# Performance work log

Measured on AMD Instinct MI355X. Metric: run time of the kernel, lower is better.

## Reference

```python
import jax, jax.numpy as jnp
import numpy as np

DIM, PATCHES, HID, NCLS, NBLK, PS = 384, 196, 1536, 1000, 24, 16

def fq(w, bits=8):
    # symmetric per-tensor fake quantization (dequantized), as in QAT DynamicQLinear
    n = float(2 ** (bits - 1) - 1)
    s = jnp.max(jnp.abs(w)) / n + 1e-8
    q = jnp.clip(jnp.round(w / s), -n - 1.0, n) * s
    return q

def setup_inputs() -> dict:
    key = jax.random.key(0)
    ks = jax.random.split(key, 12)
    d = {}
    d["x"] = jax.random.normal(ks[0], (64, 3, 224, 224), jnp.float32)
    d["conv_w"] = jax.random.normal(ks[1], (DIM, 3, PS, PS), jnp.float32) * 0.02
    d["conv_b"] = jnp.zeros((DIM,), jnp.float32)
    d["norm1_a"] = jnp.ones((NBLK, DIM), jnp.float32)
    d["norm1_b"] = jnp.zeros((NBLK, DIM), jnp.float32)
    d["attn_w"] = jax.random.normal(ks[2], (NBLK, PATCHES, PATCHES), jnp.float32) * 0.02
    d["attn_b"] = jnp.zeros((NBLK, PATCHES), jnp.float32)
    d["gamma1"] = jnp.full((NBLK, DIM), 1e-4, jnp.float32)
    d["norm2_a"] = jnp.ones((NBLK, DIM), jnp.float32)
    d["norm2_b"] = jnp.zeros((NBLK, DIM), jnp.float32)
    d["mlp_w1"] = jax.random.normal(ks[3], (NBLK, HID, DIM), jnp.float32) * 0.02
    d["mlp_b1"] = jnp.zeros((NBLK, HID), jnp.float32)
    d["mlp_w2"] = jax.random.normal(ks[4], (NBLK, DIM, HID), jnp.float32) * 0.02
    d["mlp_b2"] = jnp.zeros((NBLK, DIM), jnp.float32)
    d["gamma2"] = jnp.full((NBLK, DIM), 1e-4, jnp.float32)
    d["norm_a"] = jnp.ones((DIM,), jnp.float32)
    d["norm_b"] = jnp.zeros((DIM,), jnp.float32)
    d["head_w"] = jax.random.normal(ks[5], (NCLS, DIM), jnp.float32) * 0.02
    d["head_b"] = jnp.zeros((NCLS,), jnp.float32)
    return d

def reference(x, conv_w, conv_b, norm1_a, norm1_b, attn_w, attn_b, gamma1,
              norm2_a, norm2_b, mlp_w1, mlp_b1, mlp_w2, mlp_b2, gamma2,
              norm_a, norm_b, head_w, head_b):
    B = x.shape[0]
    # patch embed: quantized 16x16 stride-16 conv, then flatten(2).transpose(1,2)
    h = jax.lax.conv_general_dilated(x, fq(conv_w), (PS, PS), 'VALID',
                                     dimension_numbers=('NCHW', 'OIHW', 'NCHW'))
    h = h + conv_b[None, :, None, None]
    h = h.reshape(B, DIM, PATCHES).transpose(0, 2, 1)  # [B, 196, 384]

    def step(xc, p):
        a1, b1, aw, ab, g1, a2, b2, w1, bb1, w2, bb2, g2 = p
        # affine norm1 (per-channel)
        t = xc * a1 + b1
        # cross-patch linear applied on transposed layout: out[b,q,d] = sum_p t[b,p,d] W[q,p]
        t = jnp.einsum('bpd,qp->bqd', t, fq(aw)) + ab[None, :, None]
        xc = g1 * t + xc
        # affine norm2 + MLP (384 -> 1536 -> 384, exact GELU)
        t = xc * a2 + b2
        t = jax.nn.gelu(jnp.einsum('bpd,hd->bph', t, fq(w1)) + bb1, approximate=False)
        t = jnp.einsum('bph,dh->bpd', t, fq(w2)) + bb2
        xc = g2 * t + xc
        return xc, None

    h, _ = jax.lax.scan(step, h, (norm1_a, norm1_b, attn_w, attn_b, gamma1,
                                  norm2_a, norm2_b, mlp_w1, mlp_b1, mlp_w2, mlp_b2, gamma2))
    h = h * norm_a + norm_b          # final affine norm
    h = h.mean(axis=1)               # mean pool over patches -> [B, 384]
    return h @ fq(head_w).T + head_b  # [B, 1000]
```

## Files before the change

kernel.cpp:

```cpp
#include <hip/hip_runtime.h>

#define DIM 384
#define PATCHES 196
#define HID 1536
#define NBLK 24
#define NPAD 256
#define XROWS (64 * PATCHES)
#define BDCOLS (64 * DIM)
#define XELEMS (XROWS * DIM)
#define ESTRIDE 132

typedef __attribute__((ext_vector_type(8))) short s8v;
typedef __attribute__((ext_vector_type(4))) float f4v;
typedef unsigned char uchar;
typedef long long i64t;

__device__ __forceinline__ short f2bf(float f) {
  unsigned u = __float_as_uint(f);
  u += 0x7FFFu + ((u >> 16) & 1u);
  return (short)(u >> 16);
}

__device__ __forceinline__ float gelu_f(float x) {
  float u2 = 1.5957691216f * (x + 0.044715f * x * x * x);
  return x / (1.0f + __expf(-u2));
}

__device__ __forceinline__ unsigned pk4_fp8(float a, float b, float c, float d) {
  int lo = __builtin_amdgcn_cvt_pk_fp8_f32(a, b, 0, false);
  int full = __builtin_amdgcn_cvt_pk_fp8_f32(c, d, lo, true);
  return (unsigned)full;
}
__device__ __forceinline__ uchar fp8_1(float a) {
  return (uchar)(__builtin_amdgcn_cvt_pk_fp8_f32(a, a, 0, false) & 0xff);
}

__device__ __forceinline__ void gload_lds16(const void* g, void* l) {
  __builtin_amdgcn_global_load_lds((const __attribute__((address_space(1))) void*)g,
                                   (__attribute__((address_space(3))) void*)l, 16, 0, 0);
}

__global__ __launch_bounds__(256)
void absmax_v4(const float* __restrict__ src, int f4per, int blocks_per,
               unsigned* __restrict__ out) {
  int tens = blockIdx.x / blocks_per;
  int sl = blockIdx.x - tens * blocks_per;
  const float4* p = (const float4*)(src + (size_t)tens * f4per * 4);
  float m = 0.f;
  for (int i = sl * 256 + threadIdx.x; i < f4per; i += blocks_per * 256) {
    float4 v = p[i];
    m = fmaxf(m, fmaxf(fmaxf(fabsf(v.x), fabsf(v.y)), fmaxf(fabsf(v.z), fabsf(v.w))));
  }
  __shared__ float red[256];
  red[threadIdx.x] = m;
  __syncthreads();
  for (int s = 128; s > 0; s >>= 1) {
    if ((int)threadIdx.x < s) red[threadIdx.x] = fmaxf(red[threadIdx.x], red[threadIdx.x + s]);
    __syncthreads();
  }
  if (threadIdx.x == 0) atomicMax(out + tens, __float_as_uint(red[0]));
}

__global__ __launch_bounds__(256)
void quant_w(const float* __restrict__ w, short* __restrict__ q,
             const unsigned* __restrict__ sc, int per, int total) {
  int i = blockIdx.x * 256 + threadIdx.x;
  if (i >= total) return;
  int tens = i / per;
  float s = __uint_as_float(sc[tens]) / 127.0f + 1e-8f;
  float v = rintf(w[i] / s);
  v = fminf(fmaxf(v, -128.0f), 127.0f) * s;
  q[i] = f2bf(v);
}

__global__ __launch_bounds__(256)
void quant_fp8(const float* __restrict__ w, unsigned* __restrict__ q,
               const unsigned* __restrict__ sc, int per, int total4) {
  int i = blockIdx.x * 256 + threadIdx.x;
  if (i >= total4) return;
  int e = i << 2;
  int tens = e / per;
  float s = __uint_as_float(sc[tens]) / 127.0f + 1e-8f;
  float4 w4 = *(const float4*)(w + e);
  float a = fminf(fmaxf(rintf(w4.x / s), -128.0f), 127.0f) * s;
  float b = fminf(fmaxf(rintf(w4.y / s), -128.0f), 127.0f) * s;
  float c = fminf(fmaxf(rintf(w4.z / s), -128.0f), 127.0f) * s;
  float d = fminf(fmaxf(rintf(w4.w / s), -128.0f), 127.0f) * s;
  q[i] = pk4_fp8(a, b, c, d);
}

__global__ __launch_bounds__(256)
void quant_attn_fp8(const float* __restrict__ w, unsigned* __restrict__ q,
                    const unsigned* __restrict__ sc) {
  int i = blockIdx.x * 256 + threadIdx.x;
  if (i >= NBLK * PATCHES * NPAD / 4) return;
  int e = i << 2;
  int col = e & (NPAD - 1);
  int rt = e >> 8;
  int row = rt % PATCHES;
  int tens = rt / PATCHES;
  float s = __uint_as_float(sc[tens]) / 127.0f + 1e-8f;
  const float* wr = w + (size_t)tens * PATCHES * PATCHES + (size_t)row * PATCHES;
  float v[4];
#pragma unroll
  for (int k = 0; k < 4; ++k) {
    int c = col + k;
    v[k] = (c < PATCHES) ? fminf(fmaxf(rintf(wr[c] / s), -128.0f), 127.0f) * s : 0.f;
  }
  q[i] = pk4_fp8(v[0], v[1], v[2], v[3]);
}

__global__ __launch_bounds__(256)
void quant_head_v4(const float* __restrict__ w, float* __restrict__ q,
                   const unsigned* __restrict__ sc) {
  int i = blockIdx.x * 256 + threadIdx.x;
  if (i >= 1000 * DIM / 4) return;
  float s = __uint_as_float(sc[0]) / 127.0f + 1e-8f;
  float4 w4 = *(const float4*)(w + (i << 2));
  float4 o;
  o.x = fminf(fmaxf(rintf(w4.x / s), -128.0f), 127.0f) * s;
  o.y = fminf(fmaxf(rintf(w4.y / s), -128.0f), 127.0f) * s;
  o.z = fminf(fmaxf(rintf(w4.z / s), -128.0f), 127.0f) * s;
  o.w = fminf(fmaxf(rintf(w4.w / s), -128.0f), 127.0f) * s;
  *(float4*)(q + (i << 2)) = o;
}

__global__ __launch_bounds__(256)
void im2col_k(const float* __restrict__ x, short* __restrict__ Xa) {
  int idx = blockIdx.x * 256 + threadIdx.x;
  if (idx >= XROWS * 768 / 4) return;
  int e = idx << 2;
  int r = e / 768, k = e - r * 768;
  int b = r / PATCHES, p = r - b * PATCHES;
  int c = k >> 8, rem = k & 255, ii = rem >> 4, j = rem & 15;
  int ph = p / 14, pw = p - ph * 14;
  const float4 v = *(const float4*)(x + (b * 3 + c) * 50176 + (ph * 16 + ii) * 224 + pw * 16 + j);
  short2* o = (short2*)(Xa + e);
  o[0] = make_short2(f2bf(v.x), f2bf(v.y));
  o[1] = make_short2(f2bf(v.z), f2bf(v.w));
}

__global__ __launch_bounds__(256)
void gemm_conv(const short* __restrict__ A, const short* __restrict__ B,
               float* __restrict__ Xres, const float* __restrict__ bias,
               const float* __restrict__ n1a, const float* __restrict__ n1b,
               uchar* __restrict__ Yt) {
  constexpr int TILE_SHORTS = 192 * 64;
  __shared__ char smem[2 * TILE_SHORTS * 2];
  short* buf0 = (short*)smem;
  float* S = (float*)smem;
  const int lda = 768, K = 768;

  const int t = threadIdx.x;
  const int lane = t & 63;
  const int wid = t >> 6;
  const int wr = wid >> 1, wc = wid & 1;

  const int gx = gridDim.x;
  const int nwg = gx * gridDim.y;
  const int orig = blockIdx.y * gx + blockIdx.x;
  const int q = nwg >> 3, rm = nwg & 7;
  const int xc = orig & 7, jj = orig >> 3;
  const int wg = (xc < rm ? xc * (q + 1) : rm * (q + 1) + (xc - rm) * q) + jj;
  const int bx = wg % gx, by = wg / gx;
  const int m0 = by * 64, n0 = bx * 128;

  f4v acc[2][4];
#pragma unroll
  for (int m = 0; m < 2; ++m)
#pragma unroll
    for (int n = 0; n < 4; ++n) acc[m][n] = (f4v){0.f, 0.f, 0.f, 0.f};

  const int srow = t >> 3;
  const int scol = ((t & 7) ^ (srow & 7)) << 3;
  const short* ga[2];
#pragma unroll
  for (int h = 0; h < 2; ++h) ga[h] = A + (size_t)(m0 + h * 32 + srow) * lda + scol;
  const short* gb[4];
#pragma unroll
  for (int j = 0; j < 4; ++j) gb[j] = B + (size_t)(n0 + j * 32 + srow) * lda + scol;
  short* ldst = buf0 + (t & ~63) * 8;

  auto stage = [&](int slot, int kt) {
    const int koff = kt << 6;
    const int boff = slot * TILE_SHORTS;
    gload_lds16(ga[0] + koff, ldst + boff);
    gload_lds16(ga[1] + koff, ldst + boff + 2048);
#pragma unroll
    for (int j = 0; j < 4; ++j)
      gload_lds16(gb[j] + koff, ldst + boff + 4096 + j * 2048);
  };

  const int l15 = lane & 15, lk = lane >> 4, l7 = lane & 7;
  int paoff[2], pboff[2];
#pragma unroll
  for (int ks = 0; ks < 2; ++ks) {
    const int cgx = ((ks << 2) + lk) ^ l7;
    paoff[ks] = (wr * 32 + l15) * 64 + (cgx << 3);
    pboff[ks] = 4096 + (wc * 64 + l15) * 64 + (cgx << 3);
  }

  const int nk = K >> 6;
  stage(0, 0);
  asm volatile("s_waitcnt vmcnt(0)" ::: "memory");
  __builtin_amdgcn_s_barrier();
  for (int kt = 0; kt < nk; ++kt) {
    const int cur = kt & 1;
    if (kt + 1 < nk) stage(cur ^ 1, kt + 1);
    const short* base = buf0 + cur * TILE_SHORTS;
    s8v af[2][2], bfr[4][2];
#pragma unroll
    for (int m = 0; m < 2; ++m)
#pragma unroll
      for (int ks = 0; ks < 2; ++ks) af[m][ks] = *(const s8v*)(base + paoff[ks] + m * 1024);
#pragma unroll
    for (int n = 0; n < 4; ++n)
#pragma unroll
      for (int ks = 0; ks < 2; ++ks) bfr[n][ks] = *(const s8v*)(base + pboff[ks] + n * 1024);
    asm volatile("s_waitcnt lgkmcnt(0)" ::: "memory");
    __builtin_amdgcn_sched_barrier(0);
    __builtin_amdgcn_s_setprio(1);
#pragma unroll
    for (int m = 0; m < 2; ++m)
#pragma unroll
      for (int n = 0; n < 4; ++n)
#pragma unroll
        for (int ks = 0; ks < 2; ++ks)
          acc[m][n] = __builtin_amdgcn_mfma_f32_16x16x32_bf16(af[m][ks], bfr[n][ks], acc[m][n], 0, 0, 0);
    __builtin_amdgcn_s_setprio(0);
    if (kt + 1 < nk) {
      asm volatile("s_waitcnt vmcnt(0)" ::: "memory");
      __builtin_amdgcn_s_barrier();
    }
  }

  const int cb = (wc << 6) + l15;
  const int rl = t >> 3;
  const int c0 = (t & 7) << 4;
#pragma unroll
  for (int m = 0; m < 2; ++m) {
    __syncthreads();
#pragma unroll
    for (int n = 0; n < 4; ++n) {
      int c = cb + n * 16;
#pragma unroll
      for (int j = 0; j < 4; ++j)
        S[((wr << 4) + (lk << 2) + j) * ESTRIDE + c] = acc[m][n][j];
    }
    __syncthreads();
    const int r = m0 + (rl >> 4) * 32 + m * 16 + (rl & 15);
    const int colg = n0 + c0;
    float xn[16];
#pragma unroll
    for (int i = 0; i < 4; ++i) {
      float4 q4 = *(const float4*)(S + rl * ESTRIDE + c0 + i * 4);
      float4 b4 = *(const float4*)(bias + colg + i * 4);
      float4 o4 = make_float4(q4.x + b4.x, q4.y + b4.y, q4.z + b4.z, q4.w + b4.w);
      *(float4*)(Xres + (size_t)r * DIM + colg + i * 4) = o4;
      xn[4 * i] = o4.x; xn[4 * i + 1] = o4.y; xn[4 * i + 2] = o4.z; xn[4 * i + 3] = o4.w;
    }
    int bb = r / PATCHES, p = r - bb * PATCHES;
    uchar* yrow = Yt + ((size_t)(bb * DIM + colg)) * NPAD + p;
#pragma unroll
    for (int i = 0; i < 4; ++i) {
      float4 a4 = *(const float4*)(n1a + colg + i * 4);
      float4 b4 = *(const float4*)(n1b + colg + i * 4);
      yrow[(4 * i + 0) * NPAD] = fp8_1(xn[4 * i] * a4.x + b4.x);
      yrow[(4 * i + 1) * NPAD] = fp8_1(xn[4 * i + 1] * a4.y + b4.y);
      yrow[(4 * i + 2) * NPAD] = fp8_1(xn[4 * i + 2] * a4.z + b4.z);
      yrow[(4 * i + 3) * NPAD] = fp8_1(xn[4 * i + 3] * a4.w + b4.w);
    }
  }
}

template <int EPI, int NKT>
__global__ __launch_bounds__(256)
void gemm8(const uchar* __restrict__ A, int lda8, int Mlim,
           const uchar* __restrict__ B, int ldb8, int K,
           float* __restrict__ Xres, uchar* __restrict__ OutB8,
           const float* __restrict__ bias, const float* __restrict__ gamma,
           const float* __restrict__ n2a, const float* __restrict__ n2b,
           const float* __restrict__ n1a, const float* __restrict__ n1b,
           uchar* __restrict__ Yt) {
  constexpr int TILE_BYTES = 192 * 128;
  constexpr int NB = (NKT > 0) ? NKT : 2;
  __shared__ char smem[NB * TILE_BYTES];
  char* buf0 = smem;
  float* S = (float*)smem;

  const int t = threadIdx.x;
  const int lane = t & 63;
  const int wid = t >> 6;
  const int wr = wid >> 1, wc = wid & 1;

  const int gx = gridDim.x;
  const int nwg = gx * gridDim.y;
  const int orig = blockIdx.y * gx + blockIdx.x;
  const int q = nwg >> 3, rm = nwg & 7;
  const int xc = orig & 7, jj = orig >> 3;
  const int wg = (xc < rm ? xc * (q + 1) : rm * (q + 1) + (xc - rm) * q) + jj;
  const int bx = wg % gx, by = wg / gx;
  const int m0 = by * 64, n0 = bx * 128;

  f4v acc[2][4];
#pragma unroll
  for (int m = 0; m < 2; ++m)
#pragma unroll
    for (int n = 0; n < 4; ++n) acc[m][n] = (f4v){0.f, 0.f, 0.f, 0.f};

  const int srow = t >> 3;
  const int scolB = (((t & 7) ^ (srow & 7)) << 4);
  const uchar* ga[2];
#pragma unroll
  for (int h = 0; h < 2; ++h) {
    int r = m0 + h * 32 + srow;
    if (r >= Mlim) r = Mlim - 1;
    ga[h] = A + (size_t)r * lda8 + scolB;
  }
  const uchar* gb[4];
#pragma unroll
  for (int j = 0; j < 4; ++j)
    gb[j] = B + (size_t)(n0 + j * 32 + srow) * ldb8 + scolB;
  char* ldst = buf0 + (t & ~63) * 16;

  auto stage = [&](int slot, int kt) {
    const int koff = kt << 7;
    const int boff = slot * TILE_BYTES;
    gload_lds16(ga[0] + koff, ldst + boff);
    gload_lds16(ga[1] + koff, ldst + boff + 4096);
#pragma unroll
    for (int j = 0; j < 4; ++j)
      gload_lds16(gb[j] + koff, ldst + boff + 8192 + j * 4096);
  };

  const int l15 = lane & 15, lk = lane >> 4, l7 = lane & 7;
  int cterm[4];
#pragma unroll
  for (int ks = 0; ks < 4; ++ks)
    cterm[ks] = ((((ks << 1) + (lk >> 1)) ^ l7) << 4) + ((lk & 1) << 3);
  int arow[2], brow[4];
#pragma unroll
  for (int m = 0; m < 2; ++m) arow[m] = (wr * 32 + m * 16 + l15) << 7;
#pragma unroll
  for (int n = 0; n < 4; ++n) brow[n] = 8192 + ((wc * 64 + n * 16 + l15) << 7);

  if (NKT > 0) {
#pragma unroll
    for (int kt = 0; kt < NKT; ++kt) stage(kt, kt);
    __syncthreads();
#pragma unroll
    for (int kt = 0; kt < NKT; ++kt) {
      const char* base = buf0 + kt * TILE_BYTES;
      i64t af[2][4], bfr[4][4];
#pragma unroll
      for (int m = 0; m < 2; ++m)
#pragma unroll
        for (int ks = 0; ks < 4; ++ks) af[m][ks] = *(const i64t*)(base + arow[m] + cterm[ks]);
#pragma unroll
      for (int n = 0; n < 4; ++n)
#pragma unroll
        for (int ks = 0; ks < 4; ++ks) bfr[n][ks] = *(const i64t*)(base + brow[n] + cterm[ks]);
      __builtin_amdgcn_s_setprio(1);
#pragma unroll
      for (int ks = 0; ks < 4; ++ks)
#pragma unroll
        for (int m = 0; m < 2; ++m)
#pragma unroll
          for (int n = 0; n < 4; ++n)
            acc[m][n] = __builtin_amdgcn_mfma_f32_16x16x32_fp8_fp8(af[m][ks], bfr[n][ks], acc[m][n], 0, 0, 0);
      __builtin_amdgcn_s_setprio(0);
    }
  } else {
    const int nk = K >> 7;
    stage(0, 0);
    asm volatile("s_waitcnt vmcnt(0)" ::: "memory");
    __builtin_amdgcn_s_barrier();
    for (int kt = 0; kt < nk; ++kt) {
      const int cur = kt & 1;
      if (kt + 1 < nk) stage(cur ^ 1, kt + 1);
      const char* base = buf0 + cur * TILE_BYTES;
      i64t af[2][4], bfr[4][4];
#pragma unroll
      for (int m = 0; m < 2; ++m)
#pragma unroll
        for (int ks = 0; ks < 4; ++ks) af[m][ks] = *(const i64t*)(base + arow[m] + cterm[ks]);
#pragma unroll
      for (int n = 0; n < 4; ++n)
#pragma unroll
        for (int ks = 0; ks < 4; ++ks) bfr[n][ks] = *(const i64t*)(base + brow[n] + cterm[ks]);
      asm volatile("s_waitcnt lgkmcnt(0)" ::: "memory");
      __builtin_amdgcn_sched_barrier(0);
      __builtin_amdgcn_s_setprio(1);
#pragma unroll
      for (int ks = 0; ks < 4; ++ks)
#pragma unroll
        for (int m = 0; m < 2; ++m)
#pragma unroll
          for (int n = 0; n < 4; ++n)
            acc[m][n] = __builtin_amdgcn_mfma_f32_16x16x32_fp8_fp8(af[m][ks], bfr[n][ks], acc[m][n], 0, 0, 0);
      __builtin_amdgcn_s_setprio(0);
      if (kt + 1 < nk) {
        asm volatile("s_waitcnt vmcnt(0)" ::: "memory");
        __builtin_amdgcn_s_barrier();
      }
    }
  }

  const int cb = (wc << 6) + l15;
  const int rl = t >> 3;
  const int c0 = (t & 7) << 4;
#pragma unroll
  for (int m = 0; m < 2; ++m) {
    __syncthreads();
#pragma unroll
    for (int n = 0; n < 4; ++n) {
      int c = cb + n * 16;
#pragma unroll
      for (int j = 0; j < 4; ++j)
        S[((wr << 4) + (lk << 2) + j) * ESTRIDE + c] = acc[m][n][j];
    }
    __syncthreads();
    const int r = m0 + (rl >> 4) * 32 + m * 16 + (rl & 15);
    const int colg = n0 + c0;
    float v[16];
#pragma unroll
    for (int i = 0; i < 4; ++i) {
      float4 q4 = *(const float4*)(S + rl * ESTRIDE + c0 + i * 4);
      v[4 * i] = q4.x; v[4 * i + 1] = q4.y; v[4 * i + 2] = q4.z; v[4 * i + 3] = q4.w;
    }
    if (EPI == 1) {
      if (r < Mlim) {
        const int b = colg / DIM, d0 = colg - b * DIM;
        const float br = bias[r];
        const size_t base2 = (size_t)b * (PATCHES * DIM) + (size_t)r * DIM + d0;
        float xn[16];
#pragma unroll
        for (int i = 0; i < 4; ++i) {
          float4 g4 = *(const float4*)(gamma + d0 + i * 4);
          float4 x4 = *(const float4*)(Xres + base2 + i * 4);
          x4.x += g4.x * (v[4 * i] + br);
          x4.y += g4.y * (v[4 * i + 1] + br);
          x4.z += g4.z * (v[4 * i + 2] + br);
          x4.w += g4.w * (v[4 * i + 3] + br);
          *(float4*)(Xres + base2 + i * 4) = x4;
          xn[4 * i] = x4.x; xn[4 * i + 1] = x4.y; xn[4 * i + 2] = x4.z; xn[4 * i + 3] = x4.w;
        }
        unsigned o[4];
#pragma unroll
        for (int i = 0; i < 4; ++i) {
          float4 a4 = *(const float4*)(n2a + d0 + i * 4);
          float4 b4 = *(const float4*)(n2b + d0 + i * 4);
          o[i] = pk4_fp8(xn[4 * i] * a4.x + b4.x, xn[4 * i + 1] * a4.y + b4.y,
                         xn[4 * i + 2] * a4.z + b4.z, xn[4 * i + 3] * a4.w + b4.w);
        }
        *(uint4*)(OutB8 + base2) = make_uint4(o[0], o[1], o[2], o[3]);
      }
    } else if (EPI == 2) {
      unsigned o[4];
#pragma unroll
      for (int i = 0; i < 4; ++i) {
        float g0 = gelu_f(v[4 * i] + bias[colg + 4 * i]);
        float g1 = gelu_f(v[4 * i + 1] + bias[colg + 4 * i + 1]);
        float g2 = gelu_f(v[4 * i + 2] + bias[colg + 4 * i + 2]);
        float g3 = gelu_f(v[4 * i + 3] + bias[colg + 4 * i + 3]);
        o[i] = pk4_fp8(g0, g1, g2, g3);
      }
      *(uint4*)(OutB8 + (size_t)r * HID + colg) = make_uint4(o[0], o[1], o[2], o[3]);
    } else {
      float xn[16];
#pragma unroll
      for (int i = 0; i < 4; ++i) {
        float4 b4 = *(const float4*)(bias + colg + i * 4);
        float4 g4 = *(const float4*)(gamma + colg + i * 4);
        float4 x4 = *(const float4*)(Xres + (size_t)r * DIM + colg + i * 4);
        x4.x += g4.x * (v[4 * i] + b4.x);
        x4.y += g4.y * (v[4 * i + 1] + b4.y);
        x4.z += g4.z * (v[4 * i + 2] + b4.z);
        x4.w += g4.w * (v[4 * i + 3] + b4.w);
        *(float4*)(Xres + (size_t)r * DIM + colg + i * 4) = x4;
        xn[4 * i] = x4.x; xn[4 * i + 1] = x4.y; xn[4 * i + 2] = x4.z; xn[4 * i + 3] = x4.w;
      }
      if (Yt != nullptr) {
        int bb = r / PATCHES, p = r - bb * PATCHES;
        uchar* yrow = Yt + ((size_t)(bb * DIM + colg)) * NPAD + p;
#pragma unroll
        for (int i = 0; i < 4; ++i) {
          float4 a4 = *(const float4*)(n1a + colg + i * 4);
          float4 b4 = *(const float4*)(n1b + colg + i * 4);
          yrow[(4 * i + 0) * NPAD] = fp8_1(xn[4 * i] * a4.x + b4.x);
          yrow[(4 * i + 1) * NPAD] = fp8_1(xn[4 * i + 1] * a4.y + b4.y);
          yrow[(4 * i + 2) * NPAD] = fp8_1(xn[4 * i + 2] * a4.z + b4.z);
          yrow[(4 * i + 3) * NPAD] = fp8_1(xn[4 * i + 3] * a4.w + b4.w);
        }
      }
    }
  }
}

__global__ __launch_bounds__(256)
void poolnorm2(const float* __restrict__ X, const float* __restrict__ na,
               const float* __restrict__ nb, float* __restrict__ pooled) {
  __shared__ float red[4][64];
  const int b = blockIdx.x, d0 = blockIdx.y * 64;
  const int dl = threadIdx.x & 63, g = threadIdx.x >> 6;
  const float* p = X + (size_t)b * (PATCHES * DIM) + d0 + dl;
  float s = 0.f;
  for (int i = g; i < PATCHES; i += 4) s += p[(size_t)i * DIM];
  red[g][dl] = s;
  __syncthreads();
  if (threadIdx.x < 64) {
    float tot = red[0][dl] + red[1][dl] + red[2][dl] + red[3][dl];
    int d = d0 + dl;
    pooled[b * DIM + d] = (tot * (1.0f / 196.0f)) * na[d] + nb[d];
  }
}

__global__ __launch_bounds__(256)
void head_k2(const float* __restrict__ pooled, const float* __restrict__ Whq,
             const float* __restrict__ hb, float* __restrict__ out) {
  __shared__ float pl[DIM];
  const int b = blockIdx.x, t = threadIdx.x;
  if (t < 192) {
    pl[t] = pooled[b * DIM + t];
    pl[t + 192] = pooled[b * DIM + t + 192];
  }
  __syncthreads();
  const int n = blockIdx.y * 64 + (t >> 2);
  if (n >= 1000) return;
  const int qofs = (t & 3) * 96;
  const float4* w = (const float4*)(Whq + (size_t)n * DIM + qofs);
  const float* p = pl + qofs;
  float s = 0.f;
#pragma unroll 6
  for (int i = 0; i < 24; ++i) {
    float4 wv = w[i];
    s += p[4 * i] * wv.x + p[4 * i + 1] * wv.y + p[4 * i + 2] * wv.z + p[4 * i + 3] * wv.w;
  }
  s += __shfl_down(s, 2, 4);
  s += __shfl_down(s, 1, 4);
  if ((t & 3) == 0) out[b * 1000 + n] = s + hb[n];
}

extern "C" void kernel_launch(void* const* d_in, const int* in_sizes, int n_in,
                              void* d_out, int out_size, void* d_ws, size_t ws_size,
                              hipStream_t stream) {
  const float* x       = (const float*)d_in[0];
  const float* conv_w  = (const float*)d_in[1];
  const float* conv_b  = (const float*)d_in[2];
  const float* norm1_a = (const float*)d_in[3];
  const float* norm1_b = (const float*)d_in[4];
  const float* attn_w  = (const float*)d_in[5];
  const float* attn_b  = (const float*)d_in[6];
  const float* gamma1  = (const float*)d_in[7];
  const float* norm2_a = (const float*)d_in[8];
  const float* norm2_b = (const float*)d_in[9];
  const float* mlp_w1  = (const float*)d_in[10];
  const float* mlp_b1  = (const float*)d_in[11];
  const float* mlp_w2  = (const float*)d_in[12];
  const float* mlp_b2  = (const float*)d_in[13];
  const float* gamma2  = (const float*)d_in[14];
  const float* norm_a  = (const float*)d_in[15];
  const float* norm_b  = (const float*)d_in[16];
  const float* head_w  = (const float*)d_in[17];
  const float* head_b  = (const float*)d_in[18];
  (void)in_sizes; (void)n_in; (void)out_size; (void)ws_size;

  char* ws = (char*)d_ws;
  size_t off = 0;
  auto alloc = [&](size_t bytes) {
    off = (off + 255) & ~(size_t)255;
    void* p = ws + off;
    off += bytes;
    return p;
  };
  unsigned* scales = (unsigned*)alloc(74 * 4);
  short* conv_wq = (short*)alloc((size_t)DIM * 768 * 2);
  uchar* attn_wq = (uchar*)alloc((size_t)NBLK * PATCHES * NPAD);
  uchar* w1q     = (uchar*)alloc((size_t)NBLK * HID * DIM);
  uchar* w2q     = (uchar*)alloc((size_t)NBLK * DIM * HID);
  float* headq   = (float*)alloc((size_t)1000 * DIM * 4);
  float* X       = (float*)alloc((size_t)XELEMS * 4);
  uchar* Yt      = (uchar*)alloc((size_t)BDCOLS * NPAD);
  uchar* Y2      = (uchar*)alloc((size_t)XELEMS);
  uchar* H       = (uchar*)alloc((size_t)XROWS * HID);
  float* pooled  = (float*)alloc((size_t)64 * DIM * 4);
  short* Xa = (short*)H;

  hipMemsetAsync(scales, 0, 74 * 4, stream);
  hipMemsetAsync(Yt, 0, (size_t)BDCOLS * NPAD, stream);
  absmax_v4<<<32, 256, 0, stream>>>(conv_w, DIM * 768 / 4, 32, scales + 0);
  absmax_v4<<<32, 256, 0, stream>>>(head_w, 1000 * DIM / 4, 32, scales + 1);
  absmax_v4<<<NBLK * 8, 256, 0, stream>>>(attn_w, PATCHES * PATCHES / 4, 8, scales + 2);
  absmax_v4<<<NBLK * 64, 256, 0, stream>>>(mlp_w1, HID * DIM / 4, 64, scales + 26);
  absmax_v4<<<NBLK * 64, 256, 0, stream>>>(mlp_w2, DIM * HID / 4, 64, scales + 50);

  quant_w<<<(DIM * 768 + 255) / 256, 256, 0, stream>>>(conv_w, conv_wq, scales + 0, DIM * 768, DIM * 768);
  quant_fp8<<<(NBLK * HID * DIM / 4 + 255) / 256, 256, 0, stream>>>(
      mlp_w1, (unsigned*)w1q, scales + 26, HID * DIM, NBLK * HID * DIM / 4);
  quant_fp8<<<(NBLK * HID * DIM / 4 + 255) / 256, 256, 0, stream>>>(
      mlp_w2, (unsigned*)w2q, scales + 50, DIM * HID, NBLK * DIM * HID / 4);
  quant_attn_fp8<<<(NBLK * PATCHES * NPAD / 4 + 255) / 256, 256, 0, stream>>>(
      attn_w, (unsigned*)attn_wq, scales + 2);
  quant_head_v4<<<(1000 * DIM / 4 + 255) / 256, 256, 0, stream>>>(head_w, headq, scales + 1);

  im2col_k<<<(XROWS * 768 / 4) / 256, 256, 0, stream>>>(x, Xa);
  gemm_conv<<<dim3(3, 196), 256, 0, stream>>>(Xa, conv_wq, X, conv_b, norm1_a, norm1_b, Yt);

  for (int blk = 0; blk < NBLK; ++blk) {
    gemm8<1, 2><<<dim3(BDCOLS / 128, 4), 256, 0, stream>>>(
        attn_wq + (size_t)blk * PATCHES * NPAD, NPAD, PATCHES, Yt, NPAD, NPAD,
        X, Y2, attn_b + blk * PATCHES, gamma1 + blk * DIM,
        norm2_a + blk * DIM, norm2_b + blk * DIM, nullptr, nullptr, nullptr);
    gemm8<2, 3><<<dim3(HID / 128, XROWS / 64), 256, 0, stream>>>(
        Y2, DIM, XROWS, w1q + (size_t)blk * HID * DIM, DIM, DIM,
        nullptr, H, mlp_b1 + blk * HID, nullptr, nullptr, nullptr,
        nullptr, nullptr, nullptr);
    const bool last = (blk == NBLK - 1);
    gemm8<3, 0><<<dim3(DIM / 128, XROWS / 64), 256, 0, stream>>>(
        H, HID, XROWS, w2q + (size_t)blk * DIM * HID, HID, HID,
        X, nullptr, mlp_b2 + blk * DIM, gamma2 + blk * DIM, nullptr, nullptr,
        last ? nullptr : norm1_a + (blk + 1) * DIM,
        last ? nullptr : norm1_b + (blk + 1) * DIM,
        last ? nullptr : Yt);
  }

  poolnorm2<<<dim3(64, 6), 256, 0, stream>>>(X, norm_a, norm_b, pooled);
  head_k2<<<dim3(64, 16), 256, 0, stream>>>(pooled, headq, head_b, (float*)d_out);
}
```

Before: 2.144 ms.

## Use 512-thread blocks with 8 waves per 64x128 GEMM tile

```diff
diff --git a/kernel.cpp b/kernel.cpp
--- a/kernel.cpp
+++ b/kernel.cpp
@@ -273,8 +273,8 @@
   }
 }
 
-template <int EPI, int NKT>
-__global__ __launch_bounds__(256)
+template <int EPI, int NKT, int GX>
+__global__ __launch_bounds__(512)
 void gemm8(const uchar* __restrict__ A, int lda8, int Mlim,
            const uchar* __restrict__ B, int ldb8, int K,
            float* __restrict__ Xres, uchar* __restrict__ OutB8,
@@ -284,53 +284,49 @@
            uchar* __restrict__ Yt) {
   constexpr int TILE_BYTES = 192 * 128;
   constexpr int NB = (NKT > 0) ? NKT : 2;
-  __shared__ char smem[NB * TILE_BYTES];
+  constexpr int LDS_BYTES = (NB * TILE_BYTES > 64 * ESTRIDE * 4) ? NB * TILE_BYTES
+                                                                 : 64 * ESTRIDE * 4;
+  __shared__ char smem[LDS_BYTES];
   char* buf0 = smem;
   float* S = (float*)smem;
 
   const int t = threadIdx.x;
   const int lane = t & 63;
   const int wid = t >> 6;
-  const int wr = wid >> 1, wc = wid & 1;
-
-  const int gx = gridDim.x;
-  const int nwg = gx * gridDim.y;
-  const int orig = blockIdx.y * gx + blockIdx.x;
+  const int wr = wid >> 2, wc = wid & 3;
+
+  const int nwg = GX * gridDim.y;
+  const int orig = blockIdx.y * GX + blockIdx.x;
   const int q = nwg >> 3, rm = nwg & 7;
   const int xc = orig & 7, jj = orig >> 3;
   const int wg = (xc < rm ? xc * (q + 1) : rm * (q + 1) + (xc - rm) * q) + jj;
-  const int bx = wg % gx, by = wg / gx;
+  const int bx = wg % GX, by = wg / GX;
   const int m0 = by * 64, n0 = bx * 128;
 
-  f4v acc[2][4];
+  f4v acc[2][2];
 #pragma unroll
   for (int m = 0; m < 2; ++m)
 #pragma unroll
-    for (int n = 0; n < 4; ++n) acc[m][n] = (f4v){0.f, 0.f, 0.f, 0.f};
+    for (int n = 0; n < 2; ++n) acc[m][n] = (f4v){0.f, 0.f, 0.f, 0.f};
 
   const int srow = t >> 3;
   const int scolB = (((t & 7) ^ (srow & 7)) << 4);
-  const uchar* ga[2];
-#pragma unroll
-  for (int h = 0; h < 2; ++h) {
-    int r = m0 + h * 32 + srow;
-    if (r >= Mlim) r = Mlim - 1;
-    ga[h] = A + (size_t)r * lda8 + scolB;
-  }
-  const uchar* gb[4];
-#pragma unroll
-  for (int j = 0; j < 4; ++j)
-    gb[j] = B + (size_t)(n0 + j * 32 + srow) * ldb8 + scolB;
+  int ra = m0 + srow;
+  if (ra >= Mlim) ra = Mlim - 1;
+  const uchar* ga = A + (size_t)ra * lda8 + scolB;
+  const uchar* gb[2];
+#pragma unroll
+  for (int j = 0; j < 2; ++j)
+    gb[j] = B + (size_t)(n0 + j * 64 + srow) * ldb8 + scolB;
   char* ldst = buf0 + (t & ~63) * 16;
 
   auto stage = [&](int slot, int kt) {
     const int koff = kt << 7;
     const int boff = slot * TILE_BYTES;
-    gload_lds16(ga[0] + koff, ldst + boff);
-    gload_lds16(ga[1] + koff, ldst + boff + 4096);
-#pragma unroll
-    for (int j = 0; j < 4; ++j)
-      gload_lds16(gb[j] + koff, ldst + boff + 8192 + j * 4096);
+    gload_lds16(ga + koff, ldst + boff);
+#pragma unroll
+    for (int j = 0; j < 2; ++j)
+      gload_lds16(gb[j] + koff, ldst + boff + 8192 + j * 8192);
   };
 
   const int l15 = lane & 15, lk = lane >> 4, l7 = lane & 7;
@@ -338,11 +334,11 @@
 #pragma unroll
   for (int ks = 0; ks < 4; ++ks)
     cterm[ks] = ((((ks << 1) + (lk >> 1)) ^ l7) << 4) + ((lk & 1) << 3);
-  int arow[2], brow[4];
+  int arow[2], brow[2];
 #pragma unroll
   for (int m = 0; m < 2; ++m) arow[m] = (wr * 32 + m * 16 + l15) << 7;
 #pragma unroll
-  for (int n = 0; n < 4; ++n) brow[n] = 8192 + ((wc * 64 + n * 16 + l15) << 7);
+  for (int n = 0; n < 2; ++n) brow[n] = 8192 + ((wc * 32 + n * 16 + l15) << 7);
 
   if (NKT > 0) {
 #pragma unroll
@@ -351,13 +347,13 @@
 #pragma unroll
     for (int kt = 0; kt < NKT; ++kt) {
       const char* base = buf0 + kt * TILE_BYTES;
-      i64t af[2][4], bfr[4][4];
+      i64t af[2][4], bfr[2][4];
 #pragma unroll
       for (int m = 0; m < 2; ++m)
 #pragma unroll
         for (int ks = 0; ks < 4; ++ks) af[m][ks] = *(const i64t*)(base + arow[m] + cterm[ks]);
 #pragma unroll
-      for (int n = 0; n < 4; ++n)
+      for (int n = 0; n < 2; ++n)
 #pragma unroll
         for (int ks = 0; ks < 4; ++ks) bfr[n][ks] = *(const i64t*)(base + brow[n] + cterm[ks]);
       __builtin_amdgcn_s_setprio(1);
@@ -366,7 +362,7 @@
 #pragma unroll
         for (int m = 0; m < 2; ++m)
 #pragma unroll
-          for (int n = 0; n < 4; ++n)
+          for (int n = 0; n < 2; ++n)
             acc[m][n] = __builtin_amdgcn_mfma_f32_16x16x32_fp8_fp8(af[m][ks], bfr[n][ks], acc[m][n], 0, 0, 0);
       __builtin_amdgcn_s_setprio(0);
     }
@@ -379,13 +375,13 @@
       const int cur = kt & 1;
       if (kt + 1 < nk) stage(cur ^ 1, kt + 1);
       const char* base = buf0 + cur * TILE_BYTES;
-      i64t af[2][4], bfr[4][4];
+      i64t af[2][4], bfr[2][4];
 #pragma unroll
       for (int m = 0; m < 2; ++m)
 #pragma unroll
         for (int ks = 0; ks < 4; ++ks) af[m][ks] = *(const i64t*)(base + arow[m] + cterm[ks]);
 #pragma unroll
-      for (int n = 0; n < 4; ++n)
+      for (int n = 0; n < 2; ++n)
 #pragma unroll
         for (int ks = 0; ks < 4; ++ks) bfr[n][ks] = *(const i64t*)(base + brow[n] + cterm[ks]);
       asm volatile("s_waitcnt lgkmcnt(0)" ::: "memory");
@@ -396,7 +392,7 @@
 #pragma unroll
         for (int m = 0; m < 2; ++m)
 #pragma unroll
-          for (int n = 0; n < 4; ++n)
+          for (int n = 0; n < 2; ++n)
             acc[m][n] = __builtin_amdgcn_mfma_f32_16x16x32_fp8_fp8(af[m][ks], bfr[n][ks], acc[m][n], 0, 0, 0);
       __builtin_amdgcn_s_setprio(0);
       if (kt + 1 < nk) {
@@ -406,92 +402,89 @@
     }
   }
 
-  const int cb = (wc << 6) + l15;
+  __syncthreads();
+#pragma unroll
+  for (int m = 0; m < 2; ++m)
+#pragma unroll
+    for (int n = 0; n < 2; ++n) {
+      int s = wr * 32 + m * 16 + (lk << 2);
+      int c = wc * 32 + n * 16 + l15;
+#pragma unroll
+      for (int j = 0; j < 4; ++j)
+        S[(s + j) * ESTRIDE + c] = acc[m][n][j];
+    }
+  __syncthreads();
   const int rl = t >> 3;
   const int c0 = (t & 7) << 4;
-#pragma unroll
-  for (int m = 0; m < 2; ++m) {
-    __syncthreads();
-#pragma unroll
-    for (int n = 0; n < 4; ++n) {
-      int c = cb + n * 16;
-#pragma unroll
-      for (int j = 0; j < 4; ++j)
-        S[((wr << 4) + (lk << 2) + j) * ESTRIDE + c] = acc[m][n][j];
-    }
-    __syncthreads();
-    const int r = m0 + (rl >> 4) * 32 + m * 16 + (rl & 15);
-    const int colg = n0 + c0;
-    float v[16];
-#pragma unroll
-    for (int i = 0; i < 4; ++i) {
-      float4 q4 = *(const float4*)(S + rl * ESTRIDE + c0 + i * 4);
-      v[4 * i] = q4.x; v[4 * i + 1] = q4.y; v[4 * i + 2] = q4.z; v[4 * i + 3] = q4.w;
-    }
-    if (EPI == 1) {
-      if (r < Mlim) {
-        const int b = colg / DIM, d0 = colg - b * DIM;
-        const float br = bias[r];
-        const size_t base2 = (size_t)b * (PATCHES * DIM) + (size_t)r * DIM + d0;
-        float xn[16];
-#pragma unroll
-        for (int i = 0; i < 4; ++i) {
-          float4 g4 = *(const float4*)(gamma + d0 + i * 4);
-          float4 x4 = *(const float4*)(Xres + base2 + i * 4);
-          x4.x += g4.x * (v[4 * i] + br);
-          x4.y += g4.y * (v[4 * i + 1] + br);
-          x4.z += g4.z * (v[4 * i + 2] + br);
-          x4.w += g4.w * (v[4 * i + 3] + br);
-          *(float4*)(Xres + base2 + i * 4) = x4;
-          xn[4 * i] = x4.x; xn[4 * i + 1] = x4.y; xn[4 * i + 2] = x4.z; xn[4 * i + 3] = x4.w;
-        }
-        unsigned o[4];
-#pragma unroll
-        for (int i = 0; i < 4; ++i) {
-          float4 a4 = *(const float4*)(n2a + d0 + i * 4);
-          float4 b4 = *(const float4*)(n2b + d0 + i * 4);
-          o[i] = pk4_fp8(xn[4 * i] * a4.x + b4.x, xn[4 * i + 1] * a4.y + b4.y,
-                         xn[4 * i + 2] * a4.z + b4.z, xn[4 * i + 3] * a4.w + b4.w);
-        }
-        *(uint4*)(OutB8 + base2) = make_uint4(o[0], o[1], o[2], o[3]);
-      }
-    } else if (EPI == 2) {
-      unsigned o[4];
+  const int r = m0 + rl;
+  const int colg = n0 + c0;
+  float v[16];
+#pragma unroll
+  for (int i = 0; i < 4; ++i) {
+    float4 q4 = *(const float4*)(S + rl * ESTRIDE + c0 + i * 4);
+    v[4 * i] = q4.x; v[4 * i + 1] = q4.y; v[4 * i + 2] = q4.z; v[4 * i + 3] = q4.w;
+  }
+  if (EPI == 1) {
+    if (r < Mlim) {
+      const int b = colg / DIM, d0 = colg - b * DIM;
+      const float br = bias[r];
+      const size_t base2 = (size_t)b * (PATCHES * DIM) + (size_t)r * DIM + d0;
+      float xn[16];
 #pragma unroll
       for (int i = 0; i < 4; ++i) {
-        float g0 = gelu_f(v[4 * i] + bias[colg + 4 * i]);
-        float g1 = gelu_f(v[4 * i + 1] + bias[colg + 4 * i + 1]);
-        float g2 = gelu_f(v[4 * i + 2] + bias[colg + 4 * i + 2]);
-        float g3 = gelu_f(v[4 * i + 3] + bias[colg + 4 * i + 3]);
-        o[i] = pk4_fp8(g0, g1, g2, g3);
-      }
-      *(uint4*)(OutB8 + (size_t)r * HID + colg) = make_uint4(o[0], o[1], o[2], o[3]);
-    } else {
-      float xn[16];
-#pragma unroll
-      for (int i = 0; i < 4; ++i) {
-        float4 b4 = *(const float4*)(bias + colg + i * 4);
-        float4 g4 = *(const float4*)(gamma + colg + i * 4);
-        float4 x4 = *(const float4*)(Xres + (size_t)r * DIM + colg + i * 4);
-        x4.x += g4.x * (v[4 * i] + b4.x);
-        x4.y += g4.y * (v[4 * i + 1] + b4.y);
-        x4.z += g4.z * (v[4 * i + 2] + b4.z);
-        x4.w += g4.w * (v[4 * i + 3] + b4.w);
-        *(float4*)(Xres + (size_t)r * DIM + colg + i * 4) = x4;
+        float4 g4 = *(const float4*)(gamma + d0 + i * 4);
+        float4 x4 = *(const float4*)(Xres + base2 + i * 4);
+        x4.x += g4.x * (v[4 * i] + br);
+        x4.y += g4.y * (v[4 * i + 1] + br);
+        x4.z += g4.z * (v[4 * i + 2] + br);
+        x4.w += g4.w * (v[4 * i + 3] + br);
+        *(float4*)(Xres + base2 + i * 4) = x4;
         xn[4 * i] = x4.x; xn[4 * i + 1] = x4.y; xn[4 * i + 2] = x4.z; xn[4 * i + 3] = x4.w;
       }
-      if (Yt != nullptr) {
-        int bb = r / PATCHES, p = r - bb * PATCHES;
-        uchar* yrow = Yt + ((size_t)(bb * DIM + colg)) * NPAD + p;
-#pragma unroll
-        for (int i = 0; i < 4; ++i) {
-          float4 a4 = *(const float4*)(n1a + colg + i * 4);
-          float4 b4 = *(const float4*)(n1b + colg + i * 4);
-          yrow[(4 * i + 0) * NPAD] = fp8_1(xn[4 * i] * a4.x + b4.x);
-          yrow[(4 * i + 1) * NPAD] = fp8_1(xn[4 * i + 1] * a4.y + b4.y);
-          yrow[(4 * i + 2) * NPAD] = fp8_1(xn[4 * i + 2] * a4.z + b4.z);
-          yrow[(4 * i + 3) * NPAD] = fp8_1(xn[4 * i + 3] * a4.w + b4.w);
-        }
+      unsigned o[4];
+#pragma unroll
+      for (int i = 0; i < 4; ++i) {
+        float4 a4 = *(const float4*)(n2a + d0 + i * 4);
+        float4 b4 = *(const float4*)(n2b + d0 + i * 4);
+        o[i] = pk4_fp8(xn[4 * i] * a4.x + b4.x, xn[4 * i + 1] * a4.y + b4.y,
+                       xn[4 * i + 2] * a4.z + b4.z, xn[4 * i + 3] * a4.w + b4.w);
+      }
+      *(uint4*)(OutB8 + base2) = make_uint4(o[0], o[1], o[2], o[3]);
+    }
+  } else if (EPI == 2) {
+    unsigned o[4];
+#pragma unroll
+    for (int i = 0; i < 4; ++i) {
+      float4 b4 = *(const float4*)(bias + colg + i * 4);
+      o[i] = pk4_fp8(gelu_f(v[4 * i] + b4.x), gelu_f(v[4 * i + 1] + b4.y),
+                     gelu_f(v[4 * i + 2] + b4.z), gelu_f(v[4 * i + 3] + b4.w));
+    }
+    *(uint4*)(OutB8 + (size_t)r * HID + colg) = make_uint4(o[0], o[1], o[2], o[3]);
+  } else {
+    float xn[16];
+#pragma unroll
+    for (int i = 0; i < 4; ++i) {
+      float4 b4 = *(const float4*)(bias + colg + i * 4);
+      float4 g4 = *(const float4*)(gamma + colg + i * 4);
+      float4 x4 = *(const float4*)(Xres + (size_t)r * DIM + colg + i * 4);
+      x4.x += g4.x * (v[4 * i] + b4.x);
+      x4.y += g4.y * (v[4 * i + 1] + b4.y);
+      x4.z += g4.z * (v[4 * i + 2] + b4.z);
+      x4.w += g4.w * (v[4 * i + 3] + b4.w);
+      *(float4*)(Xres + (size_t)r * DIM + colg + i * 4) = x4;
+      xn[4 * i] = x4.x; xn[4 * i + 1] = x4.y; xn[4 * i + 2] = x4.z; xn[4 * i + 3] = x4.w;
+    }
+    if (Yt != nullptr) {
+      int bb = r / PATCHES, p = r - bb * PATCHES;
+      uchar* yrow = Yt + ((size_t)(bb * DIM + colg)) * NPAD + p;
+#pragma unroll
+      for (int i = 0; i < 4; ++i) {
+        float4 a4 = *(const float4*)(n1a + colg + i * 4);
+        float4 b4 = *(const float4*)(n1b + colg + i * 4);
+        yrow[(4 * i + 0) * NPAD] = fp8_1(xn[4 * i] * a4.x + b4.x);
+        yrow[(4 * i + 1) * NPAD] = fp8_1(xn[4 * i + 1] * a4.y + b4.y);
+        yrow[(4 * i + 2) * NPAD] = fp8_1(xn[4 * i + 2] * a4.z + b4.z);
+        yrow[(4 * i + 3) * NPAD] = fp8_1(xn[4 * i + 3] * a4.w + b4.w);
       }
     }
   }
@@ -607,16 +600,16 @@
   gemm_conv<<<dim3(3, 196), 256, 0, stream>>>(Xa, conv_wq, X, conv_b, norm1_a, norm1_b, Yt);
 
   for (int blk = 0; blk < NBLK; ++blk) {
-    gemm8<1, 2><<<dim3(BDCOLS / 128, 4), 256, 0, stream>>>(
+    gemm8<1, 2, 192><<<dim3(BDCOLS / 128, 4), 512, 0, stream>>>(
         attn_wq + (size_t)blk * PATCHES * NPAD, NPAD, PATCHES, Yt, NPAD, NPAD,
         X, Y2, attn_b + blk * PATCHES, gamma1 + blk * DIM,
         norm2_a + blk * DIM, norm2_b + blk * DIM, nullptr, nullptr, nullptr);
-    gemm8<2, 3><<<dim3(HID / 128, XROWS / 64), 256, 0, stream>>>(
+    gemm8<2, 3, 12><<<dim3(HID / 128, XROWS / 64), 512, 0, stream>>>(
         Y2, DIM, XROWS, w1q + (size_t)blk * HID * DIM, DIM, DIM,
         nullptr, H, mlp_b1 + blk * HID, nullptr, nullptr, nullptr,
         nullptr, nullptr, nullptr);
     const bool last = (blk == NBLK - 1);
-    gemm8<3, 0><<<dim3(DIM / 128, XROWS / 64), 256, 0, stream>>>(
+    gemm8<3, 0, 3><<<dim3(DIM / 128, XROWS / 64), 512, 0, stream>>>(
         H, HID, XROWS, w2q + (size_t)blk * DIM * HID, HID, HID,
         X, nullptr, mlp_b2 + blk * DIM, gamma2 + blk * DIM, nullptr, nullptr,
         last ? nullptr : norm1_a + (blk + 1) * DIM,
```

Measured after the change: 2.217 ms. +3.4%, slower.
